# Performance work log

Hardware: AMD Instinct MI355X
Metric: run time of the kernel (lower is better)

## Reference

```python
import jax, jax.numpy as jnp
import numpy as np
from jax import lax

B, DIM, L = 8, 512, 4096
GROUPS, NQ, CSIZE = 2, 8, 1024
DG = DIM // GROUPS


def setup_inputs() -> dict:
    key = jax.random.key(0)
    ks = jax.random.split(key, 10)
    s = 0.02
    return {
        "x": jax.random.normal(ks[0], (B, DIM, L), dtype=jnp.float32),
        "conv_enc_w": jax.random.normal(ks[1], (DIM, DIM, 3), dtype=jnp.float32) * s,
        "conv_enc_b": jnp.zeros((DIM,), jnp.float32),
        "pre_w": jax.random.normal(ks[2], (DIM, DIM), dtype=jnp.float32) * s,
        "pre_b": jnp.zeros((DIM,), jnp.float32),
        "codebooks": jax.random.normal(ks[3], (NQ, GROUPS, CSIZE, DG), dtype=jnp.float32) * s,
        "post_w": jax.random.normal(ks[4], (DIM, DIM), dtype=jnp.float32) * s,
        "post_b": jnp.zeros((DIM,), jnp.float32),
        "conv_dec_w": jax.random.normal(ks[5], (DIM, DIM, 3), dtype=jnp.float32) * s,
        "conv_dec_b": jnp.zeros((DIM,), jnp.float32),
    }


def _conv1d(x, w, b):
    # x: [b, d, l], w: [out, in, k], 'same' padding for k=3
    y = lax.conv_general_dilated(x, w, window_strides=(1,), padding=((1, 1),),
                                 dimension_numbers=("NCH", "OIH", "NCH"))
    return y + b[None, :, None]


def _grouped_residual_vq(h, codebooks):
    # h: [b, l, G, dg], codebooks: [Q, G, C, dg]
    b, l, g, dg = h.shape
    gidx = jnp.arange(g)[None, None, :]

    def step(carry, cb):
        residual, qout = carry
        # squared-euclidean argmin (||r||^2 term dropped: constant over codes)
        dots = jnp.einsum("blgd,gcd->blgc", residual, cb)
        c2 = jnp.sum(cb * cb, axis=-1)  # [g, c]
        idx = jnp.argmin(c2[None, None] - 2.0 * dots, axis=-1)  # [b, l, g]
        quant = cb[gidx, idx]  # gather -> [b, l, g, dg]
        commit = jnp.mean((residual - lax.stop_gradient(quant)) ** 2, axis=(0, 1, 3))  # [g]
        quant_st = residual + lax.stop_gradient(quant - residual)  # straight-through
        return (residual - lax.stop_gradient(quant), qout + quant_st), (idx, commit)

    (_, qout), (all_idx, all_loss) = lax.scan(step, (h, jnp.zeros_like(h)), codebooks)
    # all_idx: [Q, b, l, G] -> [G, b, l, Q]; all_loss: [Q, G] -> [G, Q]
    return qout, all_idx.transpose(3, 1, 2, 0), all_loss.T


def reference(x, conv_enc_w, conv_enc_b, pre_w, pre_b, codebooks,
              post_w, post_b, conv_dec_w, conv_dec_b):
    b, d, l = x.shape
    g = codebooks.shape[1]
    h = _conv1d(x, conv_enc_w, conv_enc_b)            # [b, d, l]
    h = h.transpose(0, 2, 1)                          # [b, l, d]
    h = h @ pre_w.T + pre_b                           # pre linear
    hg = h.reshape(b, l, g, d // g)                   # chunk dim into groups
    qout, indices, losses = _grouped_residual_vq(hg, codebooks)
    q = qout.reshape(b, l, d) @ post_w.T + post_b     # post linear
    q = q.transpose(0, 2, 1)                          # [b, d, l]
    _ = _conv1d(q, conv_dec_w, conv_dec_b)            # computed then discarded, as in original
    return (q, indices, losses)
```

## Files before the change

### kernel.cpp

```cpp
#include <hip/hip_runtime.h>
#include <cstdint>
#include <cstddef>

#define BB     8
#define DIMC   512
#define LL     4096
#define POSN   (BB*LL)
#define NG     2
#define NQ     8
#define CS     1024
#define DG     256

#define Q_OFF    0
#define IDX_OFF  16777216
#define LOSS_OFF 17301504

#define OFF_WFT   0
#define OFF_BF    786432
#define OFF_C2    786944
#define OFF_QOUT  803328
#define OFF_CANDD 17580544
#define OFF_CANDI 17842688
#define OFF_LOSSP 18104832

__global__ __launch_bounds__(256) void k_fuse_w(const float* __restrict__ cw,
                                               const float* __restrict__ prew,
                                               float* __restrict__ wft) {
    __shared__ __align__(16) float As[16][68];
    __shared__ __align__(16) float Bs[16][68];
    int bid = blockIdx.x;
    int mt = bid >> 3, nt = bid & 7;
    int m0 = mt * 64, n0 = nt * 64;
    int t = threadIdx.x, tx = t & 15, ty = t >> 4;
    float acc[4][4] = {};
    for (int k0 = 0; k0 < 512; k0 += 16) {
        for (int u = t; u < 16 * 64; u += 256) {
            int kk = u >> 6, mm = u & 63;
            As[kk][mm] = cw[(size_t)(k0 + kk) * 1536 + m0 + mm];
        }
        {
            int r = t >> 2, c4 = t & 3;
            float4 v = *(const float4*)&prew[(size_t)(n0 + r) * 512 + k0 + c4 * 4];
            Bs[c4 * 4 + 0][r] = v.x; Bs[c4 * 4 + 1][r] = v.y;
            Bs[c4 * 4 + 2][r] = v.z; Bs[c4 * 4 + 3][r] = v.w;
        }
        __syncthreads();
#pragma unroll
        for (int k = 0; k < 16; ++k) {
            float4 a = *(const float4*)&As[k][ty * 4];
            float4 b = *(const float4*)&Bs[k][tx * 4];
            float av[4] = {a.x, a.y, a.z, a.w}, bv[4] = {b.x, b.y, b.z, b.w};
#pragma unroll
            for (int i = 0; i < 4; ++i)
#pragma unroll
                for (int j = 0; j < 4; ++j) acc[i][j] += av[i] * bv[j];
        }
        __syncthreads();
    }
#pragma unroll
    for (int i = 0; i < 4; ++i) {
        float4 v = {acc[i][0], acc[i][1], acc[i][2], acc[i][3]};
        *(float4*)&wft[(size_t)(m0 + ty * 4 + i) * 512 + n0 + tx * 4] = v;
    }
}

__global__ void k_bias(const float* __restrict__ prew, const float* __restrict__ preb,
                       const float* __restrict__ ceb, float* __restrict__ bf) {
    int dd = blockIdx.x * 256 + threadIdx.x;
    if (dd < 512) {
        float s = preb[dd];
        for (int j = 0; j < 512; ++j) s += prew[(size_t)dd * 512 + j] * ceb[j];
        bf[dd] = s;
    }
}

__global__ void k_c2(const float* __restrict__ cb, float* __restrict__ c2) {
    int wave = threadIdx.x >> 6, lane = threadIdx.x & 63;
    int row = blockIdx.x * 4 + wave;
    const float* r = cb + (size_t)row * 256;
    float4 v = *(const float4*)&r[lane * 4];
    float s = v.x * v.x + v.y * v.y + v.z * v.z + v.w * v.w;
#pragma unroll
    for (int m = 1; m < 64; m <<= 1) s += __shfl_xor(s, m);
    if (lane == 0) c2[row] = s;
}

__global__ __launch_bounds__(256) void k_conv(const float* __restrict__ x,
                                              const float* __restrict__ wft,
                                              const float* __restrict__ bf,
                                              float* __restrict__ h) {
    int bid = blockIdx.x;
    int dt = bid >> 9;
    int rem = bid & 511;
    int bb = rem >> 6, lt = rem & 63;
    int l0 = lt * 64, d0 = dt * 64;
    int t = threadIdx.x, tx = t & 15, ty = t >> 4;
    __shared__ float Xs[8][68];
    __shared__ __align__(16) float Ws[24][64];
    float acc[4][4] = {};
    const float* xb = x + (size_t)bb * 512 * 4096;
    for (int i0 = 0; i0 < 512; i0 += 8) {
        for (int u = t; u < 8 * 66; u += 256) {
            int ii = u / 66, c = u % 66;
            int gl = l0 + c - 1;
            Xs[ii][c] = (gl >= 0 && gl < 4096) ? xb[(size_t)(i0 + ii) * 4096 + gl] : 0.f;
        }
        for (int u = t; u < 24 * 64; u += 256) {
            int r = u >> 6, c = u & 63;
            Ws[r][c] = wft[(size_t)(i0 * 3 + r) * 512 + d0 + c];
        }
        __syncthreads();
#pragma unroll
        for (int ii = 0; ii < 8; ++ii) {
            float a[6];
#pragma unroll
            for (int j = 0; j < 6; ++j) a[j] = Xs[ii][ty * 4 + j];
#pragma unroll
            for (int k = 0; k < 3; ++k) {
                float4 b = *(const float4*)&Ws[ii * 3 + k][tx * 4];
                float bv[4] = {b.x, b.y, b.z, b.w};
#pragma unroll
                for (int jl = 0; jl < 4; ++jl)
#pragma unroll
                    for (int jd = 0; jd < 4; ++jd) acc[jl][jd] += a[jl + k] * bv[jd];
            }
        }
        __syncthreads();
    }
    int posb = bb * 4096 + l0 + ty * 4;
    const float4 bias = *(const float4*)&bf[d0 + tx * 4];
#pragma unroll
    for (int jl = 0; jl < 4; ++jl) {
        float4 v = {acc[jl][0] + bias.x, acc[jl][1] + bias.y,
                    acc[jl][2] + bias.z, acc[jl][3] + bias.w};
        *(float4*)&h[(size_t)(posb + jl) * 512 + d0 + tx * 4] = v;
    }
}

__global__ __launch_bounds__(256) void k_dots(const float* __restrict__ hres,
                                              const float* __restrict__ cb,
                                              const float* __restrict__ c2,
                                              float* __restrict__ candd,
                                              int* __restrict__ candi,
                                              int q, int g) {
    __shared__ __align__(16) float As[16][132];
    __shared__ __align__(16) float Bs[16][132];
    __shared__ float Dd[16][128];
    __shared__ int   Di[16][128];
    int bid = blockIdx.x;
    int mt = bid >> 3, nt = bid & 7;
    int p0 = mt * 128, n0 = nt * 128;
    int t = threadIdx.x, pt = t & 15, ct = t >> 4;
    const float* cbq = cb + (size_t)(q * 2 + g) * 1024 * 256;
    const float* c2q = c2 + (q * 2 + g) * 1024;
    float acc[8][8] = {};
    for (int k0 = 0; k0 < 256; k0 += 16) {
        for (int u = t; u < 128 * 4; u += 256) {
            int r = u >> 2, c4 = u & 3;
            float4 v = *(const float4*)&hres[(size_t)(p0 + r) * 512 + g * 256 + k0 + c4 * 4];
            As[c4 * 4 + 0][r] = v.x; As[c4 * 4 + 1][r] = v.y;
            As[c4 * 4 + 2][r] = v.z; As[c4 * 4 + 3][r] = v.w;
        }
        for (int u = t; u < 128 * 4; u += 256) {
            int r = u >> 2, c4 = u & 3;
            float4 v = *(const float4*)&cbq[(size_t)(n0 + r) * 256 + k0 + c4 * 4];
            Bs[c4 * 4 + 0][r] = v.x; Bs[c4 * 4 + 1][r] = v.y;
            Bs[c4 * 4 + 2][r] = v.z; Bs[c4 * 4 + 3][r] = v.w;
        }
        __syncthreads();
#pragma unroll
        for (int k = 0; k < 16; ++k) {
            float4 a0 = *(const float4*)&As[k][pt * 8];
            float4 a1 = *(const float4*)&As[k][pt * 8 + 4];
            float4 b0 = *(const float4*)&Bs[k][ct * 8];
            float4 b1 = *(const float4*)&Bs[k][ct * 8 + 4];
            float av[8] = {a0.x, a0.y, a0.z, a0.w, a1.x, a1.y, a1.z, a1.w};
            float bv[8] = {b0.x, b0.y, b0.z, b0.w, b1.x, b1.y, b1.z, b1.w};
#pragma unroll
            for (int i = 0; i < 8; ++i)
#pragma unroll
                for (int j = 0; j < 8; ++j) acc[i][j] += av[i] * bv[j];
        }
        __syncthreads();
    }
#pragma unroll
    for (int i = 0; i < 8; ++i) {
        float bd = 1e30f; int bi = 0x7fffffff;
#pragma unroll
        for (int j = 0; j < 8; ++j) {
            int c = n0 + ct * 8 + j;
            float d = c2q[c] - 2.f * acc[i][j];
            if (d < bd) { bd = d; bi = c; }
        }
        Dd[ct][pt * 8 + i] = bd;
        Di[ct][pt * 8 + i] = bi;
    }
    __syncthreads();
    if (t < 128) {
        float bd = Dd[0][t]; int bi = Di[0][t];
#pragma unroll
        for (int j = 1; j < 16; ++j) {
            float d = Dd[j][t]; int i2 = Di[j][t];
            if (d < bd || (d == bd && i2 < bi)) { bd = d; bi = i2; }
        }
        candd[(size_t)(p0 + t) * 8 + nt] = bd;
        candi[(size_t)(p0 + t) * 8 + nt] = bi;
    }
}

__global__ __launch_bounds__(256) void k_fin(float* __restrict__ hres,
                                             const float* __restrict__ cb,
                                             const float* __restrict__ candd,
                                             const int* __restrict__ candi,
                                             float* __restrict__ qout,
                                             float* __restrict__ lossp,
                                             float* __restrict__ idx_out,
                                             int q, int g) {
    int t = threadIdx.x, wave = t >> 6, lane = t & 63;
    const float* cbq = cb + (size_t)(q * 2 + g) * 1024 * 256;
    float lsum = 0.f;
    int pbase = blockIdx.x * 32 + wave * 8;
    for (int i = 0; i < 8; ++i) {
        int pos = pbase + i;
        float bd; int bi;
        if (lane < 8) { bd = candd[(size_t)pos * 8 + lane]; bi = candi[(size_t)pos * 8 + lane]; }
        else          { bd = 1e30f; bi = 0x7fffffff; }
#pragma unroll
        for (int m = 1; m < 8; m <<= 1) {
            float d2 = __shfl_xor(bd, m);
            int   i2 = __shfl_xor(bi, m);
            if (d2 < bd || (d2 == bd && i2 < bi)) { bd = d2; bi = i2; }
        }
        int idx = __shfl(bi, 0);
        float4 cv = *(const float4*)&cbq[(size_t)idx * 256 + lane * 4];
        size_t ro = (size_t)pos * 512 + g * 256 + lane * 4;
        float4 rv = *(const float4*)&hres[ro];
        float4 rn = {rv.x - cv.x, rv.y - cv.y, rv.z - cv.z, rv.w - cv.w};
        *(float4*)&hres[ro] = rn;
        if (q == 0) {
            *(float4*)&qout[ro] = cv;
        } else {
            float4 qv = *(const float4*)&qout[ro];
            qv.x += cv.x; qv.y += cv.y; qv.z += cv.z; qv.w += cv.w;
            *(float4*)&qout[ro] = qv;
        }
        lsum += rn.x * rn.x + rn.y * rn.y + rn.z * rn.z + rn.w * rn.w;
        if (lane == 0)
            idx_out[(size_t)(g * 32768 + pos) * 8 + q] = (float)idx;
    }
#pragma unroll
    for (int m = 1; m < 64; m <<= 1) lsum += __shfl_xor(lsum, m);
    __shared__ float ls[4];
    if (lane == 0) ls[wave] = lsum;
    __syncthreads();
    if (t == 0) lossp[(size_t)(g * 8 + q) * 1024 + blockIdx.x] = ls[0] + ls[1] + ls[2] + ls[3];
}

__global__ __launch_bounds__(256) void k_post(const float* __restrict__ qout,
                                              const float* __restrict__ pw,
                                              const float* __restrict__ pb,
                                              float* __restrict__ out) {
    __shared__ __align__(16) float As[16][68];
    __shared__ __align__(16) float Bs[16][68];
    int bid = blockIdx.x;
    int mt = bid >> 3, nt = bid & 7;
    int p0 = mt * 64, d0 = nt * 64;
    int t = threadIdx.x, tx = t & 15, ty = t >> 4;
    float acc[4][4] = {};
    for (int k0 = 0; k0 < 512; k0 += 16) {
        int r = t >> 2, c4 = t & 3;
        {
            float4 v = *(const float4*)&qout[(size_t)(p0 + r) * 512 + k0 + c4 * 4];
            As[c4 * 4 + 0][r] = v.x; As[c4 * 4 + 1][r] = v.y;
            As[c4 * 4 + 2][r] = v.z; As[c4 * 4 + 3][r] = v.w;
        }
        {
            float4 v = *(const float4*)&pw[(size_t)(d0 + r) * 512 + k0 + c4 * 4];
            Bs[c4 * 4 + 0][r] = v.x; Bs[c4 * 4 + 1][r] = v.y;
            Bs[c4 * 4 + 2][r] = v.z; Bs[c4 * 4 + 3][r] = v.w;
        }
        __syncthreads();
#pragma unroll
        for (int k = 0; k < 16; ++k) {
            float4 a = *(const float4*)&As[k][tx * 4];
            float4 b = *(const float4*)&Bs[k][ty * 4];
            float av[4] = {a.x, a.y, a.z, a.w}, bv[4] = {b.x, b.y, b.z, b.w};
#pragma unroll
            for (int i = 0; i < 4; ++i)
#pragma unroll
                for (int j = 0; j < 4; ++j) acc[i][j] += av[i] * bv[j];
        }
        __syncthreads();
    }
    int bb = p0 >> 12, l0 = p0 & 4095;
#pragma unroll
    for (int jd = 0; jd < 4; ++jd) {
        int dd = d0 + ty * 4 + jd;
        float bias = pb[dd];
        float4 v = {acc[0][jd] + bias, acc[1][jd] + bias,
                    acc[2][jd] + bias, acc[3][jd] + bias};
        *(float4*)&out[((size_t)bb * 512 + dd) * 4096 + l0 + tx * 4] = v;
    }
}

__global__ void k_lossfin(const float* __restrict__ lossp, float* __restrict__ out) {
    int gq = blockIdx.x;
    float s = 0.f;
    for (int u = threadIdx.x; u < 1024; u += 256) s += lossp[(size_t)gq * 1024 + u];
    int wave = threadIdx.x >> 6, lane = threadIdx.x & 63;
#pragma unroll
    for (int m = 1; m < 64; m <<= 1) s += __shfl_xor(s, m);
    __shared__ float sh[4];
    if (lane == 0) sh[wave] = s;
    __syncthreads();
    if (threadIdx.x == 0)
        out[gq] = (sh[0] + sh[1] + sh[2] + sh[3]) * (1.f / (8.f * 4096.f * 256.f));
}

extern "C" void kernel_launch(void* const* d_in, const int* in_sizes, int n_in,
                              void* d_out, int out_size, void* d_ws, size_t ws_size,
                              hipStream_t stream) {
    (void)in_sizes; (void)n_in; (void)out_size; (void)ws_size;
    const float* x     = (const float*)d_in[0];
    const float* cew   = (const float*)d_in[1];
    const float* ceb   = (const float*)d_in[2];
    const float* prew  = (const float*)d_in[3];
    const float* preb  = (const float*)d_in[4];
    const float* cb    = (const float*)d_in[5];
    const float* postw = (const float*)d_in[6];
    const float* postb = (const float*)d_in[7];

    float* out = (float*)d_out;
    float* ws  = (float*)d_ws;
    float* wft   = ws + OFF_WFT;
    float* bf    = ws + OFF_BF;
    float* c2    = ws + OFF_C2;
    float* qout  = ws + OFF_QOUT;
    float* candd = ws + OFF_CANDD;
    int*   candi = (int*)(ws + OFF_CANDI);
    float* lossp = ws + OFF_LOSSP;
    float* h = out;

    k_fuse_w<<<192, 256, 0, stream>>>(cew, prew, wft);
    k_bias<<<2, 256, 0, stream>>>(prew, preb, ceb, bf);
    k_c2<<<4096, 256, 0, stream>>>(cb, c2);
    k_conv<<<4096, 256, 0, stream>>>(x, wft, bf, h);
    for (int q = 0; q < 8; ++q) {
        for (int g = 0; g < 2; ++g) {
            k_dots<<<2048, 256, 0, stream>>>(h, cb, c2, candd, candi, q, g);
            k_fin<<<1024, 256, 0, stream>>>(h, cb, candd, candi, qout, lossp,
                                            out + IDX_OFF, q, g);
        }
    }
    k_post<<<4096, 256, 0, stream>>>(qout, postw, postb, out);
    k_lossfin<<<16, 256, 0, stream>>>(lossp, out + LOSS_OFF);
}
```

Before: 4.893 ms.

## Use split-fp16 MFMA for codebook distances with top-4 candidates and exact fp32 rescoring

Result: slower. 5.670 ms (+15.9%).

```diff
diff --git a/kernel.cpp b/kernel.cpp
--- a/kernel.cpp
+++ b/kernel.cpp
@@ -19,9 +19,61 @@
 #define OFF_BF    786432
 #define OFF_C2    786944
 #define OFF_QOUT  803328
-#define OFF_CANDD 17580544
-#define OFF_CANDI 17842688
+#define OFF_CAND  17580544
 #define OFF_LOSSP 18104832
+#define OFF_RHI   18121216
+#define OFF_RLO   26509824
+#define OFF_CHI   34898432
+#define OFF_CLO   36995584
+
+typedef __attribute__((ext_vector_type(8)))  _Float16 half8;
+typedef __attribute__((ext_vector_type(4)))  _Float16 half4;
+typedef __attribute__((ext_vector_type(16))) float    f32x16;
+
+#define SPLIT_SCALE 64.0f
+#define DOT_ESCALE  4.8828125e-4f
+
+__device__ __forceinline__ void gl_lds16(const void* g, void* l) {
+    __builtin_amdgcn_global_load_lds(
+        (__attribute__((address_space(1))) void*)g,
+        (__attribute__((address_space(3))) void*)l, 16, 0, 0);
+}
+
+__device__ __forceinline__ bool dless(float d, int i, float dr, int ir) {
+    return d < dr || (d == dr && i < ir);
+}
+
+__device__ __forceinline__ void ins4(float d[4], int id[4], float nd, int ni) {
+    if (!dless(nd, ni, d[3], id[3])) return;
+    d[3] = nd; id[3] = ni;
+    if (dless(d[3], id[3], d[2], id[2])) {
+        float tf = d[2]; d[2] = d[3]; d[3] = tf;
+        int   ti = id[2]; id[2] = id[3]; id[3] = ti;
+    }
+    if (dless(d[2], id[2], d[1], id[1])) {
+        float tf = d[1]; d[1] = d[2]; d[2] = tf;
+        int   ti = id[1]; id[1] = id[2]; id[2] = ti;
+    }
+    if (dless(d[1], id[1], d[0], id[0])) {
+        float tf = d[0]; d[0] = d[1]; d[1] = tf;
+        int   ti = id[0]; id[0] = id[1]; id[1] = ti;
+    }
+}
+
+__device__ __forceinline__ void merge44(const float ad[4], const int ai[4],
+                                        const float bd[4], const int bi[4],
+                                        float rd[4], int ri[4]) {
+    int ia = 0, ib = 0;
+#pragma unroll
+    for (int k = 0; k < 4; ++k) {
+        float da = ad[ia], db = bd[ib];
+        int   xa = ai[ia], xb = bi[ib];
+        bool ta = dless(da, xa, db, xb);
+        rd[k] = ta ? da : db;
+        ri[k] = ta ? xa : xb;
+        if (ta) ++ia; else ++ib;
+    }
+}
 
 __global__ __launch_bounds__(256) void k_fuse_w(const float* __restrict__ cw,
                                                const float* __restrict__ prew,
@@ -85,10 +137,26 @@
     if (lane == 0) c2[row] = s;
 }
 
+__global__ void k_cbsplit(const float* __restrict__ cb,
+                          _Float16* __restrict__ chi, _Float16* __restrict__ clo) {
+    size_t i = (size_t)blockIdx.x * 256 + threadIdx.x;
+    float4 v = ((const float4*)cb)[i];
+    float sx = v.x * SPLIT_SCALE, sy = v.y * SPLIT_SCALE,
+          sz = v.z * SPLIT_SCALE, sw = v.w * SPLIT_SCALE;
+    half4 hi, lo;
+    hi[0] = (_Float16)sx; hi[1] = (_Float16)sy; hi[2] = (_Float16)sz; hi[3] = (_Float16)sw;
+    lo[0] = (_Float16)(sx - (float)hi[0]); lo[1] = (_Float16)(sy - (float)hi[1]);
+    lo[2] = (_Float16)(sz - (float)hi[2]); lo[3] = (_Float16)(sw - (float)hi[3]);
+    ((half4*)chi)[i] = hi;
+    ((half4*)clo)[i] = lo;
+}
+
 __global__ __launch_bounds__(256) void k_conv(const float* __restrict__ x,
                                               const float* __restrict__ wft,
                                               const float* __restrict__ bf,
-                                              float* __restrict__ h) {
+                                              float* __restrict__ h,
+                                              _Float16* __restrict__ rhi,
+                                              _Float16* __restrict__ rlo) {
     int bid = blockIdx.x;
     int dt = bid >> 9;
     int rem = bid & 511;
@@ -128,114 +196,201 @@
         __syncthreads();
     }
     int posb = bb * 4096 + l0 + ty * 4;
+    int gg = d0 >> 8;
+    int dgo = (d0 & 255) + tx * 4;
     const float4 bias = *(const float4*)&bf[d0 + tx * 4];
 #pragma unroll
     for (int jl = 0; jl < 4; ++jl) {
         float4 v = {acc[jl][0] + bias.x, acc[jl][1] + bias.y,
                     acc[jl][2] + bias.z, acc[jl][3] + bias.w};
         *(float4*)&h[(size_t)(posb + jl) * 512 + d0 + tx * 4] = v;
-    }
-}
-
-__global__ __launch_bounds__(256) void k_dots(const float* __restrict__ hres,
-                                              const float* __restrict__ cb,
-                                              const float* __restrict__ c2,
-                                              float* __restrict__ candd,
-                                              int* __restrict__ candi,
-                                              int q, int g) {
-    __shared__ __align__(16) float As[16][132];
-    __shared__ __align__(16) float Bs[16][132];
-    __shared__ float Dd[16][128];
-    __shared__ int   Di[16][128];
-    int bid = blockIdx.x;
-    int mt = bid >> 3, nt = bid & 7;
-    int p0 = mt * 128, n0 = nt * 128;
-    int t = threadIdx.x, pt = t & 15, ct = t >> 4;
-    const float* cbq = cb + (size_t)(q * 2 + g) * 1024 * 256;
-    const float* c2q = c2 + (q * 2 + g) * 1024;
-    float acc[8][8] = {};
-    for (int k0 = 0; k0 < 256; k0 += 16) {
-        for (int u = t; u < 128 * 4; u += 256) {
-            int r = u >> 2, c4 = u & 3;
-            float4 v = *(const float4*)&hres[(size_t)(p0 + r) * 512 + g * 256 + k0 + c4 * 4];
-            As[c4 * 4 + 0][r] = v.x; As[c4 * 4 + 1][r] = v.y;
-            As[c4 * 4 + 2][r] = v.z; As[c4 * 4 + 3][r] = v.w;
-        }
-        for (int u = t; u < 128 * 4; u += 256) {
-            int r = u >> 2, c4 = u & 3;
-            float4 v = *(const float4*)&cbq[(size_t)(n0 + r) * 256 + k0 + c4 * 4];
-            Bs[c4 * 4 + 0][r] = v.x; Bs[c4 * 4 + 1][r] = v.y;
-            Bs[c4 * 4 + 2][r] = v.z; Bs[c4 * 4 + 3][r] = v.w;
-        }
-        __syncthreads();
-#pragma unroll
-        for (int k = 0; k < 16; ++k) {
-            float4 a0 = *(const float4*)&As[k][pt * 8];
-            float4 a1 = *(const float4*)&As[k][pt * 8 + 4];
-            float4 b0 = *(const float4*)&Bs[k][ct * 8];
-            float4 b1 = *(const float4*)&Bs[k][ct * 8 + 4];
-            float av[8] = {a0.x, a0.y, a0.z, a0.w, a1.x, a1.y, a1.z, a1.w};
-            float bv[8] = {b0.x, b0.y, b0.z, b0.w, b1.x, b1.y, b1.z, b1.w};
-#pragma unroll
-            for (int i = 0; i < 8; ++i)
-#pragma unroll
-                for (int j = 0; j < 8; ++j) acc[i][j] += av[i] * bv[j];
-        }
-        __syncthreads();
-    }
-#pragma unroll
-    for (int i = 0; i < 8; ++i) {
-        float bd = 1e30f; int bi = 0x7fffffff;
-#pragma unroll
-        for (int j = 0; j < 8; ++j) {
-            int c = n0 + ct * 8 + j;
-            float d = c2q[c] - 2.f * acc[i][j];
-            if (d < bd) { bd = d; bi = c; }
-        }
-        Dd[ct][pt * 8 + i] = bd;
-        Di[ct][pt * 8 + i] = bi;
+        float sx = v.x * SPLIT_SCALE, sy = v.y * SPLIT_SCALE,
+              sz = v.z * SPLIT_SCALE, sw = v.w * SPLIT_SCALE;
+        half4 hi, lo;
+        hi[0] = (_Float16)sx; hi[1] = (_Float16)sy; hi[2] = (_Float16)sz; hi[3] = (_Float16)sw;
+        lo[0] = (_Float16)(sx - (float)hi[0]); lo[1] = (_Float16)(sy - (float)hi[1]);
+        lo[2] = (_Float16)(sz - (float)hi[2]); lo[3] = (_Float16)(sw - (float)hi[3]);
+        size_t so = ((size_t)gg * 32768 + posb + jl) * 256 + dgo;
+        *(half4*)&rhi[so] = hi;
+        *(half4*)&rlo[so] = lo;
+    }
+}
+
+__global__ __launch_bounds__(256) void k_dots_mfma(const _Float16* __restrict__ chi,
+                                                   const _Float16* __restrict__ clo,
+                                                   const _Float16* __restrict__ rhi,
+                                                   const _Float16* __restrict__ rlo,
+                                                   const float* __restrict__ c2,
+                                                   unsigned short* __restrict__ cand,
+                                                   int q, int g) {
+    __shared__ _Float16 As[8192];
+    __shared__ _Float16 Bs[8192];
+    __shared__ float c2s[128];
+    __shared__ float cd_s[2][128][4];
+    __shared__ int   ci_s[2][128][4];
+
+    const int bid = blockIdx.x;
+    const int mtile = bid & 7;
+    const int m0 = mtile * 128;
+    const int p0 = (bid >> 3) * 128;
+    const int t = threadIdx.x, w = t >> 6, lam = t & 63;
+    const int mtb = (w >> 1) * 2, ntb = (w & 1) * 2;
+
+    const size_t cboff = (size_t)(q * 2 + g) * CS * DG;
+    const _Float16* cbh = chi + cboff;
+    const _Float16* cbl = clo + cboff;
+    const _Float16* rh = rhi + (size_t)g * POSN * DG;
+    const _Float16* rl = rlo + (size_t)g * POSN * DG;
+    const float* c2q = c2 + (q * 2 + g) * CS;
+
+    if (t < 128) c2s[t] = c2q[m0 + t];
+
+    f32x16 acc[2][2];
+#pragma unroll
+    for (int i = 0; i < 2; ++i)
+#pragma unroll
+        for (int j = 0; j < 2; ++j) acc[i][j] = (f32x16)0.f;
+
+    const int srow = lam & 31, shh = lam >> 5;
+
+    for (int s = 0; s < 12; ++s) {
+        const int seg = s >> 2;
+        const int koff = (s & 3) * 64;
+        const _Float16* asrc = (seg < 2) ? cbh : cbl;
+        const _Float16* bsrc = (seg == 1) ? rl : rh;
+        size_t abase = (size_t)(m0 + w * 32 + srow) * DG + koff + shh * 8;
+        size_t bbase = (size_t)(p0 + w * 32 + srow) * DG + koff + shh * 8;
+#pragma unroll
+        for (int p = 0; p < 4; ++p) {
+            gl_lds16(asrc + abase + p * 16, &As[((w * 4 + p) * 64 + lam) * 8]);
+            gl_lds16(bsrc + bbase + p * 16, &Bs[((w * 4 + p) * 64 + lam) * 8]);
+        }
+        __syncthreads();
+#pragma unroll
+        for (int kc = 0; kc < 4; ++kc) {
+            half8 a0 = *(const half8*)&As[((mtb + 0) * 4 + kc) * 512 + lam * 8];
+            half8 a1 = *(const half8*)&As[((mtb + 1) * 4 + kc) * 512 + lam * 8];
+            half8 b0 = *(const half8*)&Bs[((ntb + 0) * 4 + kc) * 512 + lam * 8];
+            half8 b1 = *(const half8*)&Bs[((ntb + 1) * 4 + kc) * 512 + lam * 8];
+            acc[0][0] = __builtin_amdgcn_mfma_f32_32x32x16_f16(a0, b0, acc[0][0], 0, 0, 0);
+            acc[0][1] = __builtin_amdgcn_mfma_f32_32x32x16_f16(a0, b1, acc[0][1], 0, 0, 0);
+            acc[1][0] = __builtin_amdgcn_mfma_f32_32x32x16_f16(a1, b0, acc[1][0], 0, 0, 0);
+            acc[1][1] = __builtin_amdgcn_mfma_f32_32x32x16_f16(a1, b1, acc[1][1], 0, 0, 0);
+        }
+        __syncthreads();
+    }
+
+    const int col = lam & 31, kh = lam >> 5;
+#pragma unroll
+    for (int nt = 0; nt < 2; ++nt) {
+        float td[4] = {1e30f, 1e30f, 1e30f, 1e30f};
+        int   ti[4] = {0x7fffffff, 0x7fffffff, 0x7fffffff, 0x7fffffff};
+#pragma unroll
+        for (int mt = 0; mt < 2; ++mt) {
+#pragma unroll
+            for (int r = 0; r < 16; ++r) {
+                int row = (r & 3) + 8 * (r >> 2) + 4 * kh;
+                int code = (mtb + mt) * 32 + row;
+                float d = c2s[code] - acc[mt][nt][r] * DOT_ESCALE;
+                ins4(td, ti, d, m0 + code);
+            }
+        }
+        float pd[4]; int pi[4];
+#pragma unroll
+        for (int j = 0; j < 4; ++j) {
+            pd[j] = __shfl_xor(td[j], 32);
+            pi[j] = __shfl_xor(ti[j], 32);
+        }
+        float md[4]; int mi[4];
+        merge44(td, ti, pd, pi, md, mi);
+        if (kh == 0) {
+            int pc = (ntb + nt) * 32 + col;
+#pragma unroll
+            for (int j = 0; j < 4; ++j) {
+                cd_s[w >> 1][pc][j] = md[j];
+                ci_s[w >> 1][pc][j] = mi[j];
+            }
+        }
     }
     __syncthreads();
     if (t < 128) {
-        float bd = Dd[0][t]; int bi = Di[0][t];
-#pragma unroll
-        for (int j = 1; j < 16; ++j) {
-            float d = Dd[j][t]; int i2 = Di[j][t];
-            if (d < bd || (d == bd && i2 < bi)) { bd = d; bi = i2; }
-        }
-        candd[(size_t)(p0 + t) * 8 + nt] = bd;
-        candi[(size_t)(p0 + t) * 8 + nt] = bi;
+        float ad[4], bd[4]; int ai[4], bi[4];
+#pragma unroll
+        for (int j = 0; j < 4; ++j) {
+            ad[j] = cd_s[0][t][j]; ai[j] = ci_s[0][t][j];
+            bd[j] = cd_s[1][t][j]; bi[j] = ci_s[1][t][j];
+        }
+        float md[4]; int mi[4];
+        merge44(ad, ai, bd, bi, md, mi);
+        ushort4 cw;
+        cw.x = (unsigned short)mi[0]; cw.y = (unsigned short)mi[1];
+        cw.z = (unsigned short)mi[2]; cw.w = (unsigned short)mi[3];
+        *(ushort4*)&cand[(size_t)(p0 + t) * 32 + mtile * 4] = cw;
     }
 }
 
 __global__ __launch_bounds__(256) void k_fin(float* __restrict__ hres,
                                              const float* __restrict__ cb,
-                                             const float* __restrict__ candd,
-                                             const int* __restrict__ candi,
+                                             const float* __restrict__ c2,
+                                             const unsigned short* __restrict__ cand,
                                              float* __restrict__ qout,
                                              float* __restrict__ lossp,
                                              float* __restrict__ idx_out,
+                                             _Float16* __restrict__ rhi,
+                                             _Float16* __restrict__ rlo,
                                              int q, int g) {
+    __shared__ float rs[4][8][256];
+    __shared__ float ls[4];
     int t = threadIdx.x, wave = t >> 6, lane = t & 63;
-    const float* cbq = cb + (size_t)(q * 2 + g) * 1024 * 256;
+    const float* cbq = cb + (size_t)(q * 2 + g) * CS * DG;
+    const float* c2q = c2 + (q * 2 + g) * CS;
+    int pbase = blockIdx.x * 32 + wave * 8;
+
+    float4 rv[8];
+#pragma unroll
+    for (int i = 0; i < 8; ++i) {
+        size_t ro = (size_t)(pbase + i) * 512 + g * 256 + lane * 4;
+        rv[i] = *(const float4*)&hres[ro];
+        *(float4*)&rs[wave][i][lane * 4] = rv[i];
+    }
+
+    int cslot = lane & 31, posg = lane >> 5;
+    int resIdx[4];
+#pragma unroll
+    for (int p = 0; p < 4; ++p) {
+        int i = p * 2 + posg;
+        int pos = pbase + i;
+        int cidx = (int)cand[(size_t)pos * 32 + cslot];
+        const float* crow = cbq + (size_t)cidx * 256;
+        float acc = 0.f;
+#pragma unroll 8
+        for (int k4 = 0; k4 < 64; ++k4) {
+            float4 cv = *(const float4*)&crow[k4 * 4];
+            float4 rr = *(const float4*)&rs[wave][i][k4 * 4];
+            acc = fmaf(cv.x, rr.x, acc);
+            acc = fmaf(cv.y, rr.y, acc);
+            acc = fmaf(cv.z, rr.z, acc);
+            acc = fmaf(cv.w, rr.w, acc);
+        }
+        float bd = c2q[cidx] - 2.f * acc;
+        int bi = cidx;
+#pragma unroll
+        for (int m = 1; m < 32; m <<= 1) {
+            float od = __shfl_xor(bd, m);
+            int   oi = __shfl_xor(bi, m);
+            if (dless(od, oi, bd, bi)) { bd = od; bi = oi; }
+        }
+        resIdx[p] = bi;
+    }
+
     float lsum = 0.f;
-    int pbase = blockIdx.x * 32 + wave * 8;
+#pragma unroll
     for (int i = 0; i < 8; ++i) {
         int pos = pbase + i;
-        float bd; int bi;
-        if (lane < 8) { bd = candd[(size_t)pos * 8 + lane]; bi = candi[(size_t)pos * 8 + lane]; }
-        else          { bd = 1e30f; bi = 0x7fffffff; }
-#pragma unroll
-        for (int m = 1; m < 8; m <<= 1) {
-            float d2 = __shfl_xor(bd, m);
-            int   i2 = __shfl_xor(bi, m);
-            if (d2 < bd || (d2 == bd && i2 < bi)) { bd = d2; bi = i2; }
-        }
-        int idx = __shfl(bi, 0);
+        int idx = __shfl(resIdx[i >> 1], (i & 1) * 32);
         float4 cv = *(const float4*)&cbq[(size_t)idx * 256 + lane * 4];
         size_t ro = (size_t)pos * 512 + g * 256 + lane * 4;
-        float4 rv = *(const float4*)&hres[ro];
-        float4 rn = {rv.x - cv.x, rv.y - cv.y, rv.z - cv.z, rv.w - cv.w};
+        float4 rn = {rv[i].x - cv.x, rv[i].y - cv.y, rv[i].z - cv.z, rv[i].w - cv.w};
         *(float4*)&hres[ro] = rn;
         if (q == 0) {
             *(float4*)&qout[ro] = cv;
@@ -244,13 +399,24 @@
             qv.x += cv.x; qv.y += cv.y; qv.z += cv.z; qv.w += cv.w;
             *(float4*)&qout[ro] = qv;
         }
+        if (q < 7) {
+            float sx = rn.x * SPLIT_SCALE, sy = rn.y * SPLIT_SCALE,
+                  sz = rn.z * SPLIT_SCALE, sw = rn.w * SPLIT_SCALE;
+            half4 hi, lo;
+            hi[0] = (_Float16)sx; hi[1] = (_Float16)sy;
+            hi[2] = (_Float16)sz; hi[3] = (_Float16)sw;
+            lo[0] = (_Float16)(sx - (float)hi[0]); lo[1] = (_Float16)(sy - (float)hi[1]);
+            lo[2] = (_Float16)(sz - (float)hi[2]); lo[3] = (_Float16)(sw - (float)hi[3]);
+            size_t so = ((size_t)g * POSN + pos) * 256 + lane * 4;
+            *(half4*)&rhi[so] = hi;
+            *(half4*)&rlo[so] = lo;
+        }
         lsum += rn.x * rn.x + rn.y * rn.y + rn.z * rn.z + rn.w * rn.w;
         if (lane == 0)
             idx_out[(size_t)(g * 32768 + pos) * 8 + q] = (float)idx;
     }
 #pragma unroll
     for (int m = 1; m < 64; m <<= 1) lsum += __shfl_xor(lsum, m);
-    __shared__ float ls[4];
     if (lane == 0) ls[wave] = lsum;
     __syncthreads();
     if (t == 0) lossp[(size_t)(g * 8 + q) * 1024 + blockIdx.x] = ls[0] + ls[1] + ls[2] + ls[3];
@@ -336,20 +502,25 @@
     float* bf    = ws + OFF_BF;
     float* c2    = ws + OFF_C2;
     float* qout  = ws + OFF_QOUT;
-    float* candd = ws + OFF_CANDD;
-    int*   candi = (int*)(ws + OFF_CANDI);
+    unsigned short* cand = (unsigned short*)(ws + OFF_CAND);
     float* lossp = ws + OFF_LOSSP;
+    _Float16* rhi = (_Float16*)(ws + OFF_RHI);
+    _Float16* rlo = (_Float16*)(ws + OFF_RLO);
+    _Float16* chi = (_Float16*)(ws + OFF_CHI);
+    _Float16* clo = (_Float16*)(ws + OFF_CLO);
     float* h = out;
 
     k_fuse_w<<<192, 256, 0, stream>>>(cew, prew, wft);
     k_bias<<<2, 256, 0, stream>>>(prew, preb, ceb, bf);
     k_c2<<<4096, 256, 0, stream>>>(cb, c2);
-    k_conv<<<4096, 256, 0, stream>>>(x, wft, bf, h);
+    k_cbsplit<<<4096, 256, 0, stream>>>(cb, chi, clo);
+    k_conv<<<4096, 256, 0, stream>>>(x, wft, bf, h, rhi, rlo);
     for (int q = 0; q < 8; ++q) {
         for (int g = 0; g < 2; ++g) {
-            k_dots<<<2048, 256, 0, stream>>>(h, cb, c2, candd, candi, q, g);
-            k_fin<<<1024, 256, 0, stream>>>(h, cb, candd, candi, qout, lossp,
-                                            out + IDX_OFF, q, g);
+            k_dots_mfma<<<2048, 256, 0, stream>>>(chi, clo, rhi, rlo, c2,
+                                                  cand, q, g);
+            k_fin<<<1024, 256, 0, stream>>>(h, cb, c2, cand, qout, lossp,
+                                            out + IDX_OFF, rhi, rlo, q, g);
         }
     }
     k_post<<<4096, 256, 0, stream>>>(qout, postw, postb, out);
```
